# Kernel optimization log

Measured on AMD Instinct MI355X. Metric: run time of the kernel, lower is better.

The kernel has to match this reference:

```python
import jax, jax.numpy as jnp
import numpy as np

EPS = 1e-5

def mvn(feat):
    # instance norm with unbiased variance (torch .var default, correction=1)
    b, c, h, w = feat.shape
    x = feat.reshape(b, c, h * w)
    mean = x.mean(axis=2, keepdims=True)
    var = x.var(axis=2, ddof=1, keepdims=True) + EPS
    return ((x - mean) / jnp.sqrt(var)).reshape(b, c, h, w)

def conv1x1(x, w, bias):
    # x: [b,c,h,w], w: [o,c], bias: [o]
    return jnp.einsum('bchw,oc->bohw', x, w) + bias[None, :, None, None]

def setup_inputs() -> dict:
    key = jax.random.key(0)
    ks = jax.random.split(key, 10)
    C = 512
    content = jax.random.normal(ks[0], (4, C, 64, 64), dtype=jnp.float32)
    style = jax.random.normal(ks[1], (4, C, 64, 64), dtype=jnp.float32)
    s = 1.0 / np.sqrt(C)
    return {
        'content': content, 'style': style,
        'f_w': jax.random.normal(ks[2], (C, C), dtype=jnp.float32) * s,
        'f_b': jnp.zeros((C,), dtype=jnp.float32),
        'g_w': jax.random.normal(ks[3], (C, C), dtype=jnp.float32) * s,
        'g_b': jnp.zeros((C,), dtype=jnp.float32),
        'h_w': jax.random.normal(ks[4], (C, C), dtype=jnp.float32) * s,
        'h_b': jnp.zeros((C,), dtype=jnp.float32),
        'o_w': jax.random.normal(ks[5], (C, C), dtype=jnp.float32) * s,
        'o_b': jnp.zeros((C,), dtype=jnp.float32),
    }

def reference(content, style, f_w, f_b, g_w, g_b, h_w, h_b, o_w, o_b):
    b, c, hh, ww = content.shape
    F = conv1x1(mvn(content), f_w, f_b).reshape(b, c, hh * ww)   # [b,c,Nc]
    G = conv1x1(mvn(style), g_w, g_b).reshape(b, c, -1)          # [b,c,Ns]
    H = conv1x1(style, h_w, h_b).reshape(b, c, -1)               # [b,c,Ns]
    S = jnp.einsum('bcq,bcs->bqs', F, G)                          # [b,Nc,Ns]
    S = jax.nn.softmax(S, axis=-1)
    O = jnp.einsum('bcs,bqs->bcq', H, S).reshape(b, c, hh, ww)
    return conv1x1(O, o_w, o_b) + content
```

## Files before the change

### kernel.cpp

```cpp
#include <hip/hip_runtime.h>

constexpr int Cc = 512;
constexpr int Nn = 4096;
constexpr int Bb = 4;
#define EPS 1e-5f

using f16x8 = __attribute__((ext_vector_type(8))) _Float16;
using f32x4 = __attribute__((ext_vector_type(4))) float;
typedef unsigned short us;
typedef unsigned long long ull;

__device__ __forceinline__ us f2h(float f) {
    union { _Float16 h; us u; } v; v.h = (_Float16)f;
    return v.u;
}
__device__ __forceinline__ void gload_lds16(const void* g, void* l) {
    __builtin_amdgcn_global_load_lds(
        (const __attribute__((address_space(1))) void*)g,
        (__attribute__((address_space(3))) void*)l, 16, 0, 0);
}

__global__ __launch_bounds__(256) void stats2_kernel(const float* __restrict__ x0,
                                                     const float* __restrict__ x1,
                                                     float* __restrict__ mean0,
                                                     float* __restrict__ rstd0,
                                                     float* __restrict__ mean1,
                                                     float* __restrict__ rstd1) {
    int bc = blockIdx.x;
    const float* row;
    float *mean, *rstd;
    int idx;
    if (bc < Bb * Cc) { idx = bc; row = x0 + (size_t)idx * Nn; mean = mean0; rstd = rstd0; }
    else              { idx = bc - Bb * Cc; row = x1 + (size_t)idx * Nn; mean = mean1; rstd = rstd1; }
    float s = 0.f, sq = 0.f;
    for (int i = threadIdx.x * 4; i < Nn; i += 256 * 4) {
        float4 v = *reinterpret_cast<const float4*>(row + i);
        s  += v.x + v.y + v.z + v.w;
        sq += v.x*v.x + v.y*v.y + v.z*v.z + v.w*v.w;
    }
    for (int off = 32; off; off >>= 1) {
        s  += __shfl_down(s, off);
        sq += __shfl_down(sq, off);
    }
    __shared__ float ls[4], lsq[4];
    int wid = threadIdx.x >> 6;
    if ((threadIdx.x & 63) == 0) { ls[wid] = s; lsq[wid] = sq; }
    __syncthreads();
    if (threadIdx.x == 0) {
        float S  = ls[0] + ls[1] + ls[2] + ls[3];
        float SQ = lsq[0] + lsq[1] + lsq[2] + lsq[3];
        float m  = S / (float)Nn;
        float var = (SQ - S * m) / (float)(Nn - 1);
        mean[idx] = m;
        rstd[idx] = rsqrtf(var + EPS);
    }
}

__global__ __launch_bounds__(256) void pack_T(const float* __restrict__ X,
                                              const float* __restrict__ mean,
                                              const float* __restrict__ rstd,
                                              us* __restrict__ T0) {
    int b = blockIdx.z;
    int n0 = blockIdx.x * 64, c0 = blockIdx.y * 64;
    __shared__ float tile[64][65];
    const float* Xb = X + (size_t)b * Cc * Nn;
    for (int i = threadIdx.x; i < 64 * 64; i += 256) {
        int c = i >> 6, n = i & 63;
        float v = Xb[(size_t)(c0 + c) * Nn + n0 + n];
        int cg = b * Cc + c0 + c;
        tile[c][n] = (v - mean[cg]) * rstd[cg];
    }
    __syncthreads();
    us* Pb = T0 + (size_t)b * Nn * Cc;
    for (int i = threadIdx.x; i < 64 * 64; i += 256) {
        int n = i >> 6, c = i & 63;
        Pb[(size_t)(n0 + n) * Cc + c0 + c] = f2h(tile[c][n]);
    }
}

__global__ __launch_bounds__(256) void pack_style(const float* __restrict__ X,
                                                  const float* __restrict__ mean,
                                                  const float* __restrict__ rstd,
                                                  us* __restrict__ SNo,
                                                  us* __restrict__ SRo) {
    int b = blockIdx.z;
    int n0 = blockIdx.x * 64, c0 = blockIdx.y * 64;
    __shared__ float tile[64][65];
    const float* Xb = X + (size_t)b * Cc * Nn;
    for (int i = threadIdx.x; i < 64 * 64; i += 256) {
        int c = i >> 6, n = i & 63;
        tile[c][n] = Xb[(size_t)(c0 + c) * Nn + n0 + n];
    }
    __syncthreads();
    us* Nb = SNo + (size_t)b * Nn * Cc;
    us* Rb = SRo + (size_t)b * Nn * Cc;
    for (int i = threadIdx.x; i < 64 * 64; i += 256) {
        int n = i >> 6, c = i & 63;
        float raw = tile[c][n];
        int cg = b * Cc + c0 + c;
        size_t off = (size_t)(n0 + n) * Cc + c0 + c;
        Rb[off] = f2h(raw);
        Nb[off] = f2h((raw - mean[cg]) * rstd[cg]);
    }
}

__global__ __launch_bounds__(256) void pack_w(const float* __restrict__ fw, const float* __restrict__ gw,
                                              const float* __restrict__ hw, const float* __restrict__ ow,
                                              us* __restrict__ fo, us* __restrict__ go,
                                              us* __restrict__ ho, us* __restrict__ oo) {
    int i = blockIdx.x * 256 + threadIdx.x;
    if (i >= Cc * Cc) return;
    fo[i] = f2h(fw[i]);
    go[i] = f2h(gw[i]);
    ho[i] = f2h(hw[i]);
    oo[i] = f2h(ow[i]);
}

template <int EPI, int BIAS, bool RESID, int BM, int BN, int BK, int SWZ>
__global__ __launch_bounds__(256) void mfma_gemm(
    const us* __restrict__ A, int lda, long long strideA,
    const us* __restrict__ B, int ldb, long long strideB,
    void* __restrict__ out0, int ldc, long long strideC,
    const float* __restrict__ bias, const float* __restrict__ resid, long long strideR,
    int K) {
    constexpr int WM = BM / 2, WN = BN / 2;
    constexpr int MI = WM / 16, NI = WN / 16;
    constexpr int AE = BM * BK, BE = BN * BK;
    constexpr int BUFSZ = AE + BE;
    constexpr int ACH = AE / 512, BCH = BE / 512;
    __shared__ __attribute__((aligned(16))) us smem[2 * BUFSZ];

    int bz = blockIdx.z;
    const us* Ab = A + (size_t)bz * strideA;
    const us* Bbp = B + (size_t)bz * strideB;

    int bx = blockIdx.x, by = blockIdx.y;
    if constexpr (SWZ == 1) {
        int nwg = gridDim.x * gridDim.y;
        int bid = blockIdx.x + gridDim.x * blockIdx.y;
        int cpx = nwg >> 3;
        int swz = (bid & 7) * cpx + (bid >> 3);
        bx = swz % gridDim.x;
        by = swz / gridDim.x;
    } else if constexpr (SWZ == 2) {
        int bid = blockIdx.x + gridDim.x * blockIdx.y;
        int xcd = bid & 7;
        int idx = bid >> 3;
        int rpr = gridDim.y >> 2;
        int cpr = gridDim.x >> 1;
        int row0 = (xcd >> 1) * rpr;
        int col0 = (xcd & 1) * cpr;
        by = row0 + idx / cpr;
        bx = col0 + idx % cpr;
    }
    int m0 = by * BM, n0 = bx * BN;
    int tid = threadIdx.x, wave = tid >> 6, lane = tid & 63;
    int wr = wave >> 1, wc = wave & 1;
    int lr = lane & 15, lg = lane >> 4;

    auto stage = [&](int buf, int k0) {
        us* Asb = smem + buf * BUFSZ;
        us* Bsb = Asb + AE;
#pragma unroll
        for (int ch = wave; ch < ACH; ch += 4) {
            int e0 = ch * 512 + lane * 8;
            int kb = e0 / (BM * 32);
            int rem = e0 - kb * (BM * 32);
            int rr = rem >> 5;
            int gslot = ((rem & 31) >> 3) ^ ((rr >> 1) & 3);
            gload_lds16(Ab + (size_t)(m0 + rr) * lda + k0 + kb * 32 + gslot * 8,
                        Asb + ch * 512);
        }
#pragma unroll
        for (int ch = wave; ch < BCH; ch += 4) {
            int e0 = ch * 512 + lane * 8;
            int kb = e0 / (BN * 32);
            int rem = e0 - kb * (BN * 32);
            int rr = rem >> 5;
            int gslot = ((rem & 31) >> 3) ^ ((rr >> 1) & 3);
            gload_lds16(Bbp + (size_t)(n0 + rr) * ldb + k0 + kb * 32 + gslot * 8,
                        Bsb + ch * 512);
        }
    };

    f32x4 acc[MI][NI];
#pragma unroll
    for (int i = 0; i < MI; ++i)
#pragma unroll
        for (int j = 0; j < NI; ++j) acc[i][j] = (f32x4){0.f, 0.f, 0.f, 0.f};

    stage(0, 0);
    asm volatile("s_waitcnt vmcnt(0)" ::: "memory");
    __syncthreads();

    int nsteps = K / BK;
    for (int t = 0; t < nsteps; ++t) {
        int cur = t & 1;
        if (t + 1 < nsteps) stage(cur ^ 1, (t + 1) * BK);
        const us* As = smem + cur * BUFSZ;
        const us* Bs = As + AE;
#pragma unroll
        for (int kb = 0; kb < BK / 32; ++kb) {
            const us* Abase = As + kb * BM * 32;
            const us* Bbase = Bs + kb * BN * 32;
            f16x8 a[MI], b[NI];
#pragma unroll
            for (int x = 0; x < MI; ++x) {
                int row = wr * WM + x * 16 + lr;
                a[x] = *reinterpret_cast<const f16x8*>(
                    &Abase[row * 32 + ((lg ^ ((row >> 1) & 3)) << 3)]);
            }
#pragma unroll
            for (int x = 0; x < NI; ++x) {
                int row = wc * WN + x * 16 + lr;
                b[x] = *reinterpret_cast<const f16x8*>(
                    &Bbase[row * 32 + ((lg ^ ((row >> 1) & 3)) << 3)]);
            }
#pragma unroll
            for (int mi = 0; mi < MI; ++mi)
#pragma unroll
                for (int ni = 0; ni < NI; ++ni)
                    acc[mi][ni] = __builtin_amdgcn_mfma_f32_16x16x32_f16(a[mi], b[ni], acc[mi][ni], 0, 0, 0);
        }
        asm volatile("s_waitcnt vmcnt(0)" ::: "memory");
        __syncthreads();
    }

    constexpr int SP = BN + 4;
    float* sst = reinterpret_cast<float*>(smem);
    constexpr int CSEG = BN / 8;
    int rl = tid >> 3;
    int cb = (tid & 7) * CSEG;
#pragma unroll
    for (int mi = 0; mi < MI; ++mi) {
        __syncthreads();
#pragma unroll
        for (int ni = 0; ni < NI; ++ni) {
#pragma unroll
            for (int r = 0; r < 4; ++r)
                sst[(wr * 16 + lg * 4 + r) * SP + wc * WN + ni * 16 + lr] = acc[mi][ni][r];
        }
        __syncthreads();
        int grow = m0 + (rl >> 4) * WM + mi * 16 + (rl & 15);
        float bs = 0.f;
        if constexpr (BIAS == 1) bs = bias[grow];
#pragma unroll
        for (int j = 0; j < CSEG / 4; ++j) {
            int col = n0 + cb + j * 4;
            float4 v = *reinterpret_cast<const float4*>(&sst[rl * SP + cb + j * 4]);
            if constexpr (BIAS == 1) { v.x += bs; v.y += bs; v.z += bs; v.w += bs; }
            if constexpr (BIAS == 2) {
                const float4 bv = *reinterpret_cast<const float4*>(&bias[col]);
                v.x += bv.x; v.y += bv.y; v.z += bv.z; v.w += bv.w;
            }
            size_t off = (size_t)bz * strideC + (size_t)grow * ldc + col;
            if constexpr (RESID) {
                const float4 rr4 = *reinterpret_cast<const float4*>(
                    &resid[(size_t)bz * strideR + (size_t)grow * ldc + col]);
                v.x += rr4.x; v.y += rr4.y; v.z += rr4.z; v.w += rr4.w;
            }
            if constexpr (EPI == 0) {
                *reinterpret_cast<float4*>(&((float*)out0)[off]) = v;
            } else {
                ull pk = (ull)f2h(v.x) | ((ull)f2h(v.y) << 16)
                       | ((ull)f2h(v.z) << 32) | ((ull)f2h(v.w) << 48);
                *reinterpret_cast<ull*>(&((us*)out0)[off]) = pk;
            }
        }
    }
}

template <int SWZ>
__global__ __launch_bounds__(512) void mfma_gemm8w(
    const us* __restrict__ A, int lda, long long strideA,
    const us* __restrict__ B, int ldb, long long strideB,
    us* __restrict__ out0, int ldc, long long strideC,
    int K) {
    constexpr int BM = 256, BN = 256, BK = 32;
    constexpr int WM = 128, WN = 64;
    constexpr int MI = WM / 16, NI = WN / 16;
    constexpr int AE = BM * BK, BE = BN * BK;
    constexpr int BUFSZ = AE + BE;
    constexpr int ACH = AE / 512, BCH = BE / 512;
    __shared__ __attribute__((aligned(16))) us smem[2 * BUFSZ];

    int bz = blockIdx.z;
    const us* Ab = A + (size_t)bz * strideA;
    const us* Bbp = B + (size_t)bz * strideB;

    int bx = blockIdx.x, by = blockIdx.y;
    if constexpr (SWZ == 2) {
        int bid = blockIdx.x + gridDim.x * blockIdx.y;
        int xcd = bid & 7;
        int idx = bid >> 3;
        int rpr = gridDim.y >> 2;
        int cpr = gridDim.x >> 1;
        int row0 = (xcd >> 1) * rpr;
        int col0 = (xcd & 1) * cpr;
        by = row0 + idx / cpr;
        bx = col0 + idx % cpr;
    }
    int m0 = by * BM, n0 = bx * BN;
    int tid = threadIdx.x, wave = tid >> 6, lane = tid & 63;
    int wr = wave >> 2, wc = wave & 3;
    int lr = lane & 15, lg = lane >> 4;

    auto stage = [&](int buf, int k0) {
        us* Asb = smem + buf * BUFSZ;
        us* Bsb = Asb + AE;
#pragma unroll
        for (int ch = wave; ch < ACH; ch += 8) {
            int e0 = ch * 512 + lane * 8;
            int rr = e0 >> 5;
            int gslot = ((e0 & 31) >> 3) ^ ((rr >> 1) & 3);
            gload_lds16(Ab + (size_t)(m0 + rr) * lda + k0 + gslot * 8,
                        Asb + ch * 512);
        }
#pragma unroll
        for (int ch = wave; ch < BCH; ch += 8) {
            int e0 = ch * 512 + lane * 8;
            int rr = e0 >> 5;
            int gslot = ((e0 & 31) >> 3) ^ ((rr >> 1) & 3);
            gload_lds16(Bbp + (size_t)(n0 + rr) * ldb + k0 + gslot * 8,
                        Bsb + ch * 512);
        }
    };

    f32x4 acc[MI][NI];
#pragma unroll
    for (int i = 0; i < MI; ++i)
#pragma unroll
        for (int j = 0; j < NI; ++j) acc[i][j] = (f32x4){0.f, 0.f, 0.f, 0.f};

    stage(0, 0);
    asm volatile("s_waitcnt vmcnt(0)" ::: "memory");
    __syncthreads();

    int nsteps = K / BK;
    for (int t = 0; t < nsteps; ++t) {
        int cur = t & 1;
        if (t + 1 < nsteps) stage(cur ^ 1, (t + 1) * BK);
        const us* As = smem + cur * BUFSZ;
        const us* Bs = As + AE;
        f16x8 a[MI], b[NI];
#pragma unroll
        for (int x = 0; x < MI; ++x) {
            int row = wr * WM + x * 16 + lr;
            a[x] = *reinterpret_cast<const f16x8*>(
                &As[row * 32 + ((lg ^ ((row >> 1) & 3)) << 3)]);
        }
#pragma unroll
        for (int x = 0; x < NI; ++x) {
            int row = wc * WN + x * 16 + lr;
            b[x] = *reinterpret_cast<const f16x8*>(
                &Bs[row * 32 + ((lg ^ ((row >> 1) & 3)) << 3)]);
        }
#pragma unroll
        for (int mi = 0; mi < MI; ++mi)
#pragma unroll
            for (int ni = 0; ni < NI; ++ni)
                acc[mi][ni] = __builtin_amdgcn_mfma_f32_16x16x32_f16(a[mi], b[ni], acc[mi][ni], 0, 0, 0);
        asm volatile("s_waitcnt vmcnt(0)" ::: "memory");
        __syncthreads();
    }

#pragma unroll
    for (int mi = 0; mi < MI; ++mi) {
        int row = m0 + wr * WM + mi * 16 + lg * 4;
#pragma unroll
        for (int ni = 0; ni < NI; ++ni) {
            int col = n0 + wc * WN + ni * 16 + lr;
#pragma unroll
            for (int r = 0; r < 4; ++r) {
                size_t off = (size_t)bz * strideC + (size_t)(row + r) * ldc + col;
                out0[off] = f2h(acc[mi][ni][r]);
            }
        }
    }
}

__global__ __launch_bounds__(256) void softmax_kernel(us* __restrict__ S) {
    us* rowp = S + (size_t)blockIdx.y * ((size_t)Nn * Nn) + (size_t)blockIdx.x * Nn;
    f16x8* r8 = reinterpret_cast<f16x8*>(rowp);
    int t = threadIdx.x;
    float f[16];
    float mx = -1e30f;
#pragma unroll
    for (int j = 0; j < 2; ++j) {
        f16x8 v = r8[t + 256 * j];
#pragma unroll
        for (int e = 0; e < 8; ++e) {
            f[j * 8 + e] = (float)v[e];
            mx = fmaxf(mx, f[j * 8 + e]);
        }
    }
    for (int off = 32; off; off >>= 1) mx = fmaxf(mx, __shfl_down(mx, off));
    __shared__ float redm[4], reds[4];
    int wid = t >> 6;
    if ((t & 63) == 0) redm[wid] = mx;
    __syncthreads();
    mx = fmaxf(fmaxf(redm[0], redm[1]), fmaxf(redm[2], redm[3]));
    float s = 0.f;
#pragma unroll
    for (int j = 0; j < 16; ++j) {
        f[j] = __expf(f[j] - mx);
        s += f[j];
    }
    for (int off = 32; off; off >>= 1) s += __shfl_down(s, off);
    if ((t & 63) == 0) reds[wid] = s;
    __syncthreads();
    s = reds[0] + reds[1] + reds[2] + reds[3];
    float inv = 1.f / s;
#pragma unroll
    for (int j = 0; j < 2; ++j) {
        f16x8 o;
#pragma unroll
        for (int e = 0; e < 8; ++e) o[e] = (_Float16)(f[j * 8 + e] * inv);
        r8[t + 256 * j] = o;
    }
}

extern "C" void kernel_launch(void* const* d_in, const int* in_sizes, int n_in,
                              void* d_out, int out_size, void* d_ws, size_t ws_size,
                              hipStream_t stream) {
    const float* content = (const float*)d_in[0];
    const float* style   = (const float*)d_in[1];
    const float* f_w = (const float*)d_in[2];
    const float* f_b = (const float*)d_in[3];
    const float* g_w = (const float*)d_in[4];
    const float* g_b = (const float*)d_in[5];
    const float* h_w = (const float*)d_in[6];
    const float* h_b = (const float*)d_in[7];
    const float* o_w = (const float*)d_in[8];
    const float* o_b = (const float*)d_in[9];
    float* out = (float*)d_out;
    char* ws = (char*)d_ws;

    const size_t PB   = (size_t)Cc * Nn;
    const size_t TEN  = PB * Bb;
    const size_t SMAT = (size_t)Nn * Nn;

    us* FT  = (us*)ws;
    us* GT  = FT + TEN;
    us* Hbf = GT + TEN;
    us* OT  = Hbf + TEN;
    us* fwh = OT + TEN;
    us* gwh = fwh + Cc * Cc;
    us* hwb = gwh + Cc * Cc;
    us* owb = hwb + Cc * Cc;
    float* meanC = (float*)(owb + Cc * Cc);
    float* rstdC = meanC + Bb * Cc;
    float* meanS = rstdC + Bb * Cc;
    float* rstdS = meanS + Bb * Cc;
    us* CN = (us*)(rstdS + Bb * Cc);
    us* SN = CN + TEN;
    us* SR = SN + TEN;
    us* S4 = CN;

    stats2_kernel<<<2 * Bb * Cc, 256, 0, stream>>>(content, style,
                                                   meanC, rstdC, meanS, rstdS);

    dim3 pgrid(Nn / 64, Cc / 64, Bb);
    pack_T<<<pgrid, 256, 0, stream>>>(content, meanC, rstdC, CN);
    pack_style<<<pgrid, 256, 0, stream>>>(style, meanS, rstdS, SN, SR);
    pack_w<<<(Cc * Cc + 255) / 256, 256, 0, stream>>>(f_w, g_w, h_w, o_w,
                                                      fwh, gwh, hwb, owb);

    mfma_gemm<1, 2, false, 64, 64, 64, 1><<<dim3(Cc / 64, Nn / 64, Bb), 256, 0, stream>>>(
        CN, Cc, (long long)PB, fwh, Cc, 0,
        FT, Cc, (long long)PB, f_b, nullptr, 0, Cc);
    mfma_gemm<1, 2, false, 64, 64, 64, 1><<<dim3(Cc / 64, Nn / 64, Bb), 256, 0, stream>>>(
        SN, Cc, (long long)PB, gwh, Cc, 0,
        GT, Cc, (long long)PB, g_b, nullptr, 0, Cc);
    mfma_gemm<1, 1, false, 64, 64, 64, 1><<<dim3(Nn / 64, Cc / 64, Bb), 256, 0, stream>>>(
        hwb, Cc, 0, SR, Cc, (long long)PB,
        Hbf, Nn, (long long)PB, h_b, nullptr, 0, Cc);

    mfma_gemm8w<2><<<dim3(Nn / 256, Nn / 256, Bb), 512, 0, stream>>>(
        FT, Cc, (long long)PB, GT, Cc, (long long)PB,
        S4, Nn, (long long)SMAT, Cc);
    softmax_kernel<<<dim3(Nn, Bb), 256, 0, stream>>>(S4);
    mfma_gemm<1, 0, false, 128, 128, 64, 2><<<dim3(Cc / 128, Nn / 128, Bb), 256, 0, stream>>>(
        S4, Nn, (long long)SMAT, Hbf, Nn, (long long)PB,
        OT, Cc, (long long)PB, nullptr, nullptr, 0, Nn);

    mfma_gemm<0, 1, true, 64, 64, 64, 1><<<dim3(Nn / 64, Cc / 64, Bb), 256, 0, stream>>>(
        owb, Cc, 0, OT, Cc, (long long)PB,
        out, Nn, (long long)PB, o_b, content, (long long)PB, Cc);
}
```

Before: 326.4 us.

## Triple-buffer GEMM LDS pipeline with partial vmcnt waits and smaller BK

Both GEMM kernels move from double to triple buffering of shared memory. Tiles are now prefetched two steps ahead, and each step waits only for the oldest outstanding global-to-LDS loads using partial s_waitcnt vmcnt counts, with raw s_barrier calls in place of a full drain plus __syncthreads. BK drops from 64 to 32 for the 256-thread GEMMs so the three buffers fit in LDS. This aims to hide global load latency behind MFMA work, at the cost of more loop iterations and barriers and a dependence on exact vmcnt bookkeeping being correct.

```diff
diff --git a/kernel.cpp b/kernel.cpp
--- a/kernel.cpp
+++ b/kernel.cpp
@@ -19,6 +19,14 @@
         (const __attribute__((address_space(1))) void*)g,
         (__attribute__((address_space(3))) void*)l, 16, 0, 0);
 }
+template <int N> __device__ __forceinline__ void wait_vmcnt() {
+    if constexpr (N == 0)      asm volatile("s_waitcnt vmcnt(0)" ::: "memory");
+    else if constexpr (N == 2) asm volatile("s_waitcnt vmcnt(2)" ::: "memory");
+    else if constexpr (N == 4) asm volatile("s_waitcnt vmcnt(4)" ::: "memory");
+    else if constexpr (N == 8) asm volatile("s_waitcnt vmcnt(8)" ::: "memory");
+    else                       asm volatile("s_waitcnt vmcnt(16)" ::: "memory");
+}
+__device__ __forceinline__ void cfence() { asm volatile("" ::: "memory"); }
 
 __global__ __launch_bounds__(256) void stats2_kernel(const float* __restrict__ x0,
                                                      const float* __restrict__ x1,
@@ -128,7 +136,8 @@
     constexpr int AE = BM * BK, BE = BN * BK;
     constexpr int BUFSZ = AE + BE;
     constexpr int ACH = AE / 512, BCH = BE / 512;
-    __shared__ __attribute__((aligned(16))) us smem[2 * BUFSZ];
+    constexpr int LPT = (ACH + BCH) / 4;
+    __shared__ __attribute__((aligned(16))) us smem[3 * BUFSZ];
 
     int bz = blockIdx.z;
     const us* Ab = A + (size_t)bz * strideA;
@@ -189,15 +198,22 @@
 #pragma unroll
         for (int j = 0; j < NI; ++j) acc[i][j] = (f32x4){0.f, 0.f, 0.f, 0.f};
 
+    int nsteps = K / BK;
     stage(0, 0);
-    asm volatile("s_waitcnt vmcnt(0)" ::: "memory");
-    __syncthreads();
-
-    int nsteps = K / BK;
+    if (nsteps > 1) stage(1, BK);
+
     for (int t = 0; t < nsteps; ++t) {
-        int cur = t & 1;
-        if (t + 1 < nsteps) stage(cur ^ 1, (t + 1) * BK);
-        const us* As = smem + cur * BUFSZ;
+        if (t + 2 < nsteps) {
+            stage((t + 2) % 3, (t + 2) * BK);
+            wait_vmcnt<2 * LPT>();
+        } else if (t + 1 < nsteps) {
+            wait_vmcnt<LPT>();
+        } else {
+            wait_vmcnt<0>();
+        }
+        __builtin_amdgcn_s_barrier();
+        cfence();
+        const us* As = smem + (t % 3) * BUFSZ;
         const us* Bs = As + AE;
 #pragma unroll
         for (int kb = 0; kb < BK / 32; ++kb) {
@@ -222,8 +238,8 @@
                 for (int ni = 0; ni < NI; ++ni)
                     acc[mi][ni] = __builtin_amdgcn_mfma_f32_16x16x32_f16(a[mi], b[ni], acc[mi][ni], 0, 0, 0);
         }
-        asm volatile("s_waitcnt vmcnt(0)" ::: "memory");
-        __syncthreads();
+        __builtin_amdgcn_s_barrier();
+        cfence();
     }
 
     constexpr int SP = BN + 4;
@@ -282,7 +298,8 @@
     constexpr int AE = BM * BK, BE = BN * BK;
     constexpr int BUFSZ = AE + BE;
     constexpr int ACH = AE / 512, BCH = BE / 512;
-    __shared__ __attribute__((aligned(16))) us smem[2 * BUFSZ];
+    constexpr int LPT = (ACH + BCH) / 8;
+    __shared__ __attribute__((aligned(16))) us smem[3 * BUFSZ];
 
     int bz = blockIdx.z;
     const us* Ab = A + (size_t)bz * strideA;
@@ -332,15 +349,22 @@
 #pragma unroll
         for (int j = 0; j < NI; ++j) acc[i][j] = (f32x4){0.f, 0.f, 0.f, 0.f};
 
+    int nsteps = K / BK;
     stage(0, 0);
-    asm volatile("s_waitcnt vmcnt(0)" ::: "memory");
-    __syncthreads();
-
-    int nsteps = K / BK;
+    if (nsteps > 1) stage(1, BK);
+
     for (int t = 0; t < nsteps; ++t) {
-        int cur = t & 1;
-        if (t + 1 < nsteps) stage(cur ^ 1, (t + 1) * BK);
-        const us* As = smem + cur * BUFSZ;
+        if (t + 2 < nsteps) {
+            stage((t + 2) % 3, (t + 2) * BK);
+            wait_vmcnt<2 * LPT>();
+        } else if (t + 1 < nsteps) {
+            wait_vmcnt<LPT>();
+        } else {
+            wait_vmcnt<0>();
+        }
+        __builtin_amdgcn_s_barrier();
+        cfence();
+        const us* As = smem + (t % 3) * BUFSZ;
         const us* Bs = As + AE;
         f16x8 a[MI], b[NI];
 #pragma unroll
@@ -360,8 +384,8 @@
 #pragma unroll
             for (int ni = 0; ni < NI; ++ni)
                 acc[mi][ni] = __builtin_amdgcn_mfma_f32_16x16x32_f16(a[mi], b[ni], acc[mi][ni], 0, 0, 0);
-        asm volatile("s_waitcnt vmcnt(0)" ::: "memory");
-        __syncthreads();
+        __builtin_amdgcn_s_barrier();
+        cfence();
     }
 
 #pragma unroll
@@ -466,13 +490,13 @@
     pack_w<<<(Cc * Cc + 255) / 256, 256, 0, stream>>>(f_w, g_w, h_w, o_w,
                                                       fwh, gwh, hwb, owb);
 
-    mfma_gemm<1, 2, false, 64, 64, 64, 1><<<dim3(Cc / 64, Nn / 64, Bb), 256, 0, stream>>>(
+    mfma_gemm<1, 2, false, 64, 64, 32, 1><<<dim3(Cc / 64, Nn / 64, Bb), 256, 0, stream>>>(
         CN, Cc, (long long)PB, fwh, Cc, 0,
         FT, Cc, (long long)PB, f_b, nullptr, 0, Cc);
-    mfma_gemm<1, 2, false, 64, 64, 64, 1><<<dim3(Cc / 64, Nn / 64, Bb), 256, 0, stream>>>(
+    mfma_gemm<1, 2, false, 64, 64, 32, 1><<<dim3(Cc / 64, Nn / 64, Bb), 256, 0, stream>>>(
         SN, Cc, (long long)PB, gwh, Cc, 0,
         GT, Cc, (long long)PB, g_b, nullptr, 0, Cc);
-    mfma_gemm<1, 1, false, 64, 64, 64, 1><<<dim3(Nn / 64, Cc / 64, Bb), 256, 0, stream>>>(
+    mfma_gemm<1, 1, false, 64, 64, 32, 1><<<dim3(Nn / 64, Cc / 64, Bb), 256, 0, stream>>>(
         hwb, Cc, 0, SR, Cc, (long long)PB,
         Hbf, Nn, (long long)PB, h_b, nullptr, 0, Cc);
 
@@ -480,11 +504,11 @@
         FT, Cc, (long long)PB, GT, Cc, (long long)PB,
         S4, Nn, (long long)SMAT, Cc);
     softmax_kernel<<<dim3(Nn, Bb), 256, 0, stream>>>(S4);
-    mfma_gemm<1, 0, false, 128, 128, 64, 2><<<dim3(Cc / 128, Nn / 128, Bb), 256, 0, stream>>>(
+    mfma_gemm<1, 0, false, 128, 128, 32, 2><<<dim3(Cc / 128, Nn / 128, Bb), 256, 0, stream>>>(
         S4, Nn, (long long)SMAT, Hbf, Nn, (long long)PB,
         OT, Cc, (long long)PB, nullptr, nullptr, 0, Nn);
 
-    mfma_gemm<0, 1, true, 64, 64, 64, 1><<<dim3(Nn / 64, Cc / 64, Bb), 256, 0, stream>>>(
+    mfma_gemm<0, 1, true, 64, 64, 32, 1><<<dim3(Nn / 64, Cc / 64, Bb), 256, 0, stream>>>(
         owb, Cc, 0, OT, Cc, (long long)PB,
         out, Nn, (long long)PB, o_b, content, (long long)PB, Cc);
 }
```

New measurement: 340.5 us. 1.04x slower.
